# Optimization experiments

Hardware: AMD Instinct MI355X
Metric: run time of the kernel (lower is better)

## Reference

```python
import jax, jax.numpy as jnp
import numpy as np

B, S, D, H = 4, 2048, 1024, 16
DH = D // H


def setup_inputs() -> dict:
    key = jax.random.key(0)
    k1, k2, k3 = jax.random.split(key, 3)
    x = jax.random.normal(k1, (B, S, D), dtype=jnp.float32)
    w_attn = jax.random.normal(k2, (D, 3 * D), dtype=jnp.float32) * 0.02
    b_attn = jnp.zeros((3 * D,), dtype=jnp.float32)
    w_proj = jax.random.normal(k3, (D, D), dtype=jnp.float32) * 0.02
    b_proj = jnp.zeros((D,), dtype=jnp.float32)
    return {"x": x, "w_attn": w_attn, "b_attn": b_attn, "w_proj": w_proj, "b_proj": b_proj}


def _split_heads(t):
    # [B, S, D] -> [B, H, S, DH]
    return t.reshape(B, S, H, DH).transpose(0, 2, 1, 3)


def reference(x, w_attn, b_attn, w_proj, b_proj):
    # fused QKV projection (TFConv1D = x @ w + b)
    qkv = jnp.einsum('bsd,df->bsf', x, w_attn) + b_attn  # [B, S, 3D]
    q, k, v = jnp.split(qkv, 3, axis=2)
    q, k, v = _split_heads(q), _split_heads(k), _split_heads(v)  # [B,H,S,DH]

    # scaled scores
    w = jnp.einsum('bhqd,bhkd->bhqk', q, k) / jnp.sqrt(jnp.asarray(DH, dtype=q.dtype))

    # causal mask: multiply + additive -10000 trick, as in original
    i = jnp.arange(S)[:, None]
    j = jnp.arange(S)[None, :]
    b = (i >= j).astype(w.dtype)  # nd == ns so i >= j - ns + nd == i >= j
    b = b[None, None]  # [1,1,S,S]
    w = w * b - 10000.0 * (1.0 - b)

    w = jax.nn.softmax(w, axis=-1)
    # attn_pdrop = 0.0 -> dropout is identity (eval)

    a = jnp.einsum('bhqk,bhkd->bhqd', w, v)  # [B,H,S,DH]
    a = a.transpose(0, 2, 1, 3).reshape(B, S, D)  # merge heads
    a = jnp.einsum('bsd,df->bsf', a, w_proj) + b_proj
    # resid_pdrop = 0.0 -> identity
    return a
```

## Files before the change

### kernel.cpp

```cpp
#include <hip/hip_runtime.h>
#include <stdint.h>

typedef __bf16 bf16x8 __attribute__((ext_vector_type(8)));
typedef float  f32x4  __attribute__((ext_vector_type(4)));

#define DEV __device__ __forceinline__

constexpr int Bc = 4, S = 2048, D = 1024, Hh = 16, DH = 64;
constexpr int Kdim = 1024;

DEV unsigned short f2bf(float f) {
    uint32_t u = __builtin_bit_cast(uint32_t, f);
    u += 0x7fff + ((u >> 16) & 1);
    return (unsigned short)(u >> 16);
}
DEV bf16x8 ld8(const unsigned short* p) {
    uint4 u = *(const uint4*)p;
    return __builtin_bit_cast(bf16x8, u);
}
DEV uint4 pack8(float4 a, float4 b) {
    union { uint4 u; unsigned short s[8]; } r;
    r.s[0] = f2bf(a.x); r.s[1] = f2bf(a.y); r.s[2] = f2bf(a.z); r.s[3] = f2bf(a.w);
    r.s[4] = f2bf(b.x); r.s[5] = f2bf(b.y); r.s[6] = f2bf(b.z); r.s[7] = f2bf(b.w);
    return r.u;
}

DEV void gl16(const void* g, void* l) {
    __builtin_amdgcn_global_load_lds((__attribute__((address_space(1))) void*)g,
                                     (__attribute__((address_space(3))) void*)l,
                                     16, 0, 0);
}

__global__ __launch_bounds__(256) void transpose_cvt(const float* __restrict__ in,
                                                     unsigned short* __restrict__ out,
                                                     int rows, int cols) {
    __shared__ float t[32][33];
    int tx = threadIdx.x & 31, ty = threadIdx.x >> 5;
    int c = blockIdx.x * 32 + tx;
    int rbase = blockIdx.y * 32;
    for (int rr = 0; rr < 32; rr += 8)
        t[ty + rr][tx] = in[(size_t)(rbase + ty + rr) * cols + c];
    __syncthreads();
    int orbase = blockIdx.x * 32;
    for (int rr = 0; rr < 32; rr += 8)
        out[(size_t)(orbase + ty + rr) * rows + rbase + tx] = f2bf(t[tx][ty + rr]);
}

__global__ __launch_bounds__(256) void cvt_bf16(const float* __restrict__ in,
                                                unsigned short* __restrict__ out) {
    size_t i = (size_t)blockIdx.x * 256 + threadIdx.x;
    const float4* p = (const float4*)(in + i * 8);
    float4 a = p[0], b = p[1];
    *(uint4*)(out + i * 8) = pack8(a, b);
}

__global__ __launch_bounds__(256) void gemm_bt(const unsigned short* __restrict__ A,
                                               const unsigned short* __restrict__ Bt,
                                               const float* __restrict__ bias,
                                               int mode,
                                               unsigned short* __restrict__ qo,
                                               unsigned short* __restrict__ ko,
                                               unsigned short* __restrict__ vo,
                                               float* __restrict__ outf) {
    __shared__ __align__(16) unsigned short As[128 * 64];
    __shared__ __align__(16) unsigned short Bs[128 * 64];
    const int tid = threadIdx.x;
    const int wave = tid >> 6, lane = tid & 63, g = lane >> 4, ln = lane & 15;
    const int wm = wave >> 1, wn = wave & 1;
    const int nwg = gridDim.x * gridDim.y;
    const int orig = blockIdx.y * gridDim.x + blockIdx.x;
    const int swz = (orig & 7) * (nwg >> 3) + (orig >> 3);
    const int m0 = (swz / gridDim.x) * 128, n0 = (swz % gridDim.x) * 128;

    f32x4 acc[4][4];
    for (int i = 0; i < 4; i++)
        for (int j = 0; j < 4; j++) acc[i][j] = f32x4{0.f, 0.f, 0.f, 0.f};

    for (int k0 = 0; k0 < Kdim; k0 += 64) {
#pragma unroll
        for (int c = 0; c < 4; c++) {
            int L = c * 4096 + tid * 16;
            int row = L >> 7;
            int colb = (L & 127) ^ ((row & 7) << 4);
            gl16((const char*)A  + ((size_t)(m0 + row) * Kdim + k0) * 2 + colb,
                 (char*)As + c * 4096 + wave * 1024);
            gl16((const char*)Bt + ((size_t)(n0 + row) * Kdim + k0) * 2 + colb,
                 (char*)Bs + c * 4096 + wave * 1024);
        }
        __syncthreads();
#pragma unroll
        for (int kk = 0; kk < 2; kk++) {
            bf16x8 af[4], bfr[4];
#pragma unroll
            for (int t = 0; t < 4; t++) {
                int ra = wm * 64 + t * 16 + ln;
                int rb = wn * 64 + t * 16 + ln;
                int co = kk * 64 + g * 16;
                af[t]  = ld8((const unsigned short*)((const char*)As + ra * 128 + (co ^ ((ra & 7) << 4))));
                bfr[t] = ld8((const unsigned short*)((const char*)Bs + rb * 128 + (co ^ ((rb & 7) << 4))));
            }
#pragma unroll
            for (int mt = 0; mt < 4; mt++)
#pragma unroll
                for (int nt = 0; nt < 4; nt++)
                    acc[mt][nt] = __builtin_amdgcn_mfma_f32_16x16x32_bf16(af[mt], bfr[nt], acc[mt][nt], 0, 0, 0);
        }
        __syncthreads();
    }

    for (int mt = 0; mt < 4; mt++)
        for (int nt = 0; nt < 4; nt++)
            for (int r = 0; r < 4; r++) {
                int m = m0 + wm * 64 + mt * 16 + g * 4 + r;
                int n = n0 + wn * 64 + nt * 16 + ln;
                float val = acc[mt][nt][r] + bias[n];
                if (mode == 0) {
                    int which = n >> 10, rem = n & 1023;
                    int hh = rem >> 6, dd = rem & 63;
                    int b = m >> 11, s = m & 2047;
                    int bh = (b << 4) + hh;
                    if (which == 0)      qo[((size_t)bh * S + s) * DH + dd] = f2bf(val);
                    else if (which == 1) ko[((size_t)bh * S + s) * DH + dd] = f2bf(val);
                    else                 vo[((size_t)bh * DH + dd) * S + s] = f2bf(val);
                } else {
                    outf[(size_t)m * 1024 + n] = val;
                }
            }
}

__global__ __launch_bounds__(256, 3) void attn_fwd(const unsigned short* __restrict__ qg,
                                                   const unsigned short* __restrict__ kg,
                                                   const unsigned short* __restrict__ vtg,
                                                   unsigned short* __restrict__ og) {
    __shared__ __align__(16) unsigned short Ks[128 * 64];
    __shared__ __align__(16) unsigned short Vs[64 * 128];
    __shared__ __align__(16) unsigned short P [64 * 136];
    const int idx = blockIdx.x;
    const int qt = 31 - (idx >> 6);
    const int bh = idx & 63;
    const int b = bh >> 4, h = bh & 15;
    const size_t base = (size_t)bh * S * DH;
    const unsigned short* qp = qg + base;
    const char* kpb  = (const char*)(kg  + base);
    const char* vtpb = (const char*)(vtg + base);
    const int tid = threadIdx.x, wave = tid >> 6, lane = tid & 63;
    const int g = lane >> 4, ln = lane & 15;
    const int q0 = qt * 64, wq = wave * 16;
    const int jn = (qt >> 1) + 1;

    bf16x8 qf[2];
    qf[0] = ld8(qp + (size_t)(q0 + wq + ln) * DH + g * 8);
    qf[1] = ld8(qp + (size_t)(q0 + wq + ln) * DH + 32 + g * 8);

    f32x4 o_t[4];
#pragma unroll
    for (int dt = 0; dt < 4; dt++) o_t[dt] = f32x4{0.f, 0.f, 0.f, 0.f};
    float m_ = -1e30f, l_ = 0.f;

#pragma unroll 1
    for (int j = 0; j < jn; j++) {
        const char* kj = kpb + (size_t)j * (128 * DH * 2);
        const char* vj = vtpb + j * 256;
#pragma unroll
        for (int c = 0; c < 4; c++) {
            int L = c * 4096 + tid * 16;
            int kr = L >> 7, kcb = L & 127;
            gl16(kj + (size_t)kr * 128 + (kcb ^ ((kr & 7) << 4)),
                 (char*)Ks + c * 4096 + wave * 1024);
            int vr = L >> 8, vcb = L & 255;
            gl16(vj + (size_t)vr * 4096 + (vcb ^ ((vr & 15) << 4)),
                 (char*)Vs + c * 4096 + wave * 1024);
        }
        __syncthreads();

        f32x4 st[8];
#pragma unroll
        for (int mt = 0; mt < 8; mt++) {
            int row = mt * 16 + ln;
            int sw = (row & 7) << 4;
            const char* kb2 = (const char*)Ks + row * 128;
            bf16x8 kf0 = ld8((const unsigned short*)(kb2 + ((g * 16) ^ sw)));
            bf16x8 kf1 = ld8((const unsigned short*)(kb2 + ((64 + g * 16) ^ sw)));
            f32x4 t = f32x4{0.f, 0.f, 0.f, 0.f};
            t = __builtin_amdgcn_mfma_f32_16x16x32_bf16(kf0, qf[0], t, 0, 0, 0);
            t = __builtin_amdgcn_mfma_f32_16x16x32_bf16(kf1, qf[1], t, 0, 0, 0);
            st[mt] = t;
        }
        if (j == jn - 1) {
            int qgl = q0 + wq + ln;
#pragma unroll
            for (int mt = 0; mt < 8; mt++)
#pragma unroll
                for (int r = 0; r < 4; r++) {
                    int kvg = j * 128 + mt * 16 + g * 4 + r;
                    if (kvg > qgl) st[mt][r] = -3e38f;
                }
        }
        f32x4 mm = st[0];
#pragma unroll
        for (int mt = 1; mt < 8; mt++)
#pragma unroll
            for (int e = 0; e < 4; e++) mm[e] = fmaxf(mm[e], st[mt][e]);
        float mx = fmaxf(fmaxf(mm[0], mm[1]), fmaxf(mm[2], mm[3]));
        mx = fmaxf(mx, __shfl_xor(mx, 16));
        mx = fmaxf(mx, __shfl_xor(mx, 32));
        float mnew = fmaxf(m_, mx);
        float alpha = __expf((m_ - mnew) * 0.125f);
        f32x4 sv = f32x4{0.f, 0.f, 0.f, 0.f};
#pragma unroll
        for (int mt = 0; mt < 8; mt++) {
            f32x4 pr;
#pragma unroll
            for (int e = 0; e < 4; e++) pr[e] = __expf((st[mt][e] - mnew) * 0.125f);
            st[mt] = pr;
            sv += pr;
        }
        float rs = (sv[0] + sv[1]) + (sv[2] + sv[3]);
        rs += __shfl_xor(rs, 16);
        rs += __shfl_xor(rs, 32);
        l_ = l_ * alpha + rs;
        m_ = mnew;

#pragma unroll
        for (int mt = 0; mt < 8; mt++) {
            uint4 u = __builtin_bit_cast(uint4, st[mt]);
            uint2 w;
            w.x = (u.y & 0xFFFF0000u) | (u.x >> 16);
            w.y = (u.w & 0xFFFF0000u) | (u.z >> 16);
            *(uint2*)&P[(wq + ln) * 136 + mt * 16 + g * 4] = w;
        }
#pragma unroll
        for (int dt = 0; dt < 4; dt++) o_t[dt] *= alpha;

#pragma unroll
        for (int kc = 0; kc < 4; kc++) {
            bf16x8 pf = ld8(&P[(wq + ln) * 136 + kc * 32 + g * 8]);
            bf16x8 vf[4];
#pragma unroll
            for (int dt = 0; dt < 4; dt++) {
                int row = dt * 16 + ln;
                vf[dt] = ld8((const unsigned short*)((const char*)Vs + row * 256 +
                             ((kc * 64 + g * 16) ^ ((row & 15) << 4))));
            }
#pragma unroll
            for (int dt = 0; dt < 4; dt++)
                o_t[dt] = __builtin_amdgcn_mfma_f32_16x16x32_bf16(vf[dt], pf, o_t[dt], 0, 0, 0);
        }
        __syncthreads();
    }

    float il = 1.f / l_;
#pragma unroll
    for (int dt = 0; dt < 4; dt++) o_t[dt] *= il;
    float* Ot = (float*)&P[wq * 136];
#pragma unroll
    for (int dt = 0; dt < 4; dt++)
        *(float4*)&Ot[ln * 68 + dt * 16 + g * 4] =
            float4{o_t[dt][0], o_t[dt][1], o_t[dt][2], o_t[dt][3]};
#pragma unroll
    for (int i = 0; i < 4; i++) {
        float4 v = *(float4*)&Ot[(i * 4 + g) * 68 + ln * 4];
        uint2 w;
        w.x = (uint32_t)f2bf(v.x) | ((uint32_t)f2bf(v.y) << 16);
        w.y = (uint32_t)f2bf(v.z) | ((uint32_t)f2bf(v.w) << 16);
        *(uint2*)&og[((size_t)(b * S + q0 + wq + i * 4 + g)) * D + h * DH + ln * 4] = w;
    }
}

extern "C" void kernel_launch(void* const* d_in, const int* in_sizes, int n_in,
                              void* d_out, int out_size, void* d_ws, size_t ws_size,
                              hipStream_t stream) {
    (void)in_sizes; (void)n_in; (void)out_size; (void)ws_size;
    const float* x      = (const float*)d_in[0];
    const float* w_attn = (const float*)d_in[1];
    const float* b_attn = (const float*)d_in[2];
    const float* w_proj = (const float*)d_in[3];
    const float* b_proj = (const float*)d_in[4];

    char* ws = (char*)d_ws;
    unsigned short* wattn_t = (unsigned short*)ws;
    unsigned short* wproj_t = (unsigned short*)(ws + 6291456);
    unsigned short* xb      = (unsigned short*)(ws + 8388608);
    unsigned short* qb      = (unsigned short*)(ws + 25165824);
    unsigned short* kb      = (unsigned short*)(ws + 41943040);
    unsigned short* vtb     = (unsigned short*)(ws + 58720256);
    unsigned short* aob     = (unsigned short*)(ws + 75497472);

    transpose_cvt<<<dim3(96, 32), 256, 0, stream>>>(w_attn, wattn_t, 1024, 3072);
    transpose_cvt<<<dim3(32, 32), 256, 0, stream>>>(w_proj, wproj_t, 1024, 1024);
    cvt_bf16<<<dim3(4096), 256, 0, stream>>>(x, xb);
    gemm_bt<<<dim3(24, 64), 256, 0, stream>>>(xb, wattn_t, b_attn, 0, qb, kb, vtb, nullptr);
    attn_fwd<<<dim3(2048), 256, 0, stream>>>(qb, kb, vtb, aob);
    gemm_bt<<<dim3(8, 64), 256, 0, stream>>>(aob, wproj_t, b_proj, 1,
                                             nullptr, nullptr, nullptr, (float*)d_out);
}
```

Measured before the change: 284.0 us.

## Double-buffer GEMM LDS tiles and widen attention blocks to 128 queries

The GEMM kernel now keeps two LDS buffers and issues the global-to-LDS loads for the next K slice before computing on the current one. This hides load latency behind the MFMAs and leaves one barrier per iteration. The attention kernel moves to 512 threads with 128-row query tiles, so each K/V tile load is shared by twice as many queries and the grid is halved. The costs are doubled LDS use in the GEMM, a larger P buffer, fewer attention blocks, and coarser causal tiles that may compute more masked work.

```diff
diff --git a/kernel.cpp b/kernel.cpp
--- a/kernel.cpp
+++ b/kernel.cpp
@@ -62,8 +62,8 @@
                                                unsigned short* __restrict__ ko,
                                                unsigned short* __restrict__ vo,
                                                float* __restrict__ outf) {
-    __shared__ __align__(16) unsigned short As[128 * 64];
-    __shared__ __align__(16) unsigned short Bs[128 * 64];
+    __shared__ __align__(16) unsigned short As[2][128 * 64];
+    __shared__ __align__(16) unsigned short Bs[2][128 * 64];
     const int tid = threadIdx.x;
     const int wave = tid >> 6, lane = tid & 63, g = lane >> 4, ln = lane & 15;
     const int wm = wave >> 1, wn = wave & 1;
@@ -76,28 +76,39 @@
     for (int i = 0; i < 4; i++)
         for (int j = 0; j < 4; j++) acc[i][j] = f32x4{0.f, 0.f, 0.f, 0.f};
 
-    for (int k0 = 0; k0 < Kdim; k0 += 64) {
-#pragma unroll
-        for (int c = 0; c < 4; c++) {
-            int L = c * 4096 + tid * 16;
-            int row = L >> 7;
-            int colb = (L & 127) ^ ((row & 7) << 4);
-            gl16((const char*)A  + ((size_t)(m0 + row) * Kdim + k0) * 2 + colb,
-                 (char*)As + c * 4096 + wave * 1024);
-            gl16((const char*)Bt + ((size_t)(n0 + row) * Kdim + k0) * 2 + colb,
-                 (char*)Bs + c * 4096 + wave * 1024);
-        }
-        __syncthreads();
+#define STAGE_G(buf, k0)                                                            \
+    _Pragma("unroll")                                                               \
+    for (int c = 0; c < 4; c++) {                                                   \
+        int L = c * 4096 + tid * 16;                                                \
+        int row = L >> 7;                                                           \
+        int colb = (L & 127) ^ ((row & 7) << 4);                                    \
+        gl16((const char*)A  + ((size_t)(m0 + row) * Kdim + (k0)) * 2 + colb,       \
+             (char*)As[buf] + c * 4096 + wave * 1024);                              \
+        gl16((const char*)Bt + ((size_t)(n0 + row) * Kdim + (k0)) * 2 + colb,       \
+             (char*)Bs[buf] + c * 4096 + wave * 1024);                              \
+    }
+
+    STAGE_G(0, 0);
+    asm volatile("s_waitcnt vmcnt(0)" ::: "memory");
+    __builtin_amdgcn_s_barrier();
+    asm volatile("" ::: "memory");
+
+#pragma unroll 1
+    for (int t = 0; t < 16; t++) {
+        const int buf = t & 1;
+        if (t + 1 < 16) STAGE_G(buf ^ 1, (t + 1) * 64);
+        const unsigned short* Asb = As[buf];
+        const unsigned short* Bsb = Bs[buf];
 #pragma unroll
         for (int kk = 0; kk < 2; kk++) {
             bf16x8 af[4], bfr[4];
 #pragma unroll
-            for (int t = 0; t < 4; t++) {
-                int ra = wm * 64 + t * 16 + ln;
-                int rb = wn * 64 + t * 16 + ln;
+            for (int u = 0; u < 4; u++) {
+                int ra = wm * 64 + u * 16 + ln;
+                int rb = wn * 64 + u * 16 + ln;
                 int co = kk * 64 + g * 16;
-                af[t]  = ld8((const unsigned short*)((const char*)As + ra * 128 + (co ^ ((ra & 7) << 4))));
-                bfr[t] = ld8((const unsigned short*)((const char*)Bs + rb * 128 + (co ^ ((rb & 7) << 4))));
+                af[u]  = ld8((const unsigned short*)((const char*)Asb + ra * 128 + (co ^ ((ra & 7) << 4))));
+                bfr[u] = ld8((const unsigned short*)((const char*)Bsb + rb * 128 + (co ^ ((rb & 7) << 4))));
             }
 #pragma unroll
             for (int mt = 0; mt < 4; mt++)
@@ -105,8 +116,12 @@
                 for (int nt = 0; nt < 4; nt++)
                     acc[mt][nt] = __builtin_amdgcn_mfma_f32_16x16x32_bf16(af[mt], bfr[nt], acc[mt][nt], 0, 0, 0);
         }
-        __syncthreads();
+        asm volatile("" ::: "memory");
+        asm volatile("s_waitcnt vmcnt(0)" ::: "memory");
+        __builtin_amdgcn_s_barrier();
+        asm volatile("" ::: "memory");
     }
+#undef STAGE_G
 
     for (int mt = 0; mt < 4; mt++)
         for (int nt = 0; nt < 4; nt++)
@@ -128,15 +143,15 @@
             }
 }
 
-__global__ __launch_bounds__(256, 3) void attn_fwd(const unsigned short* __restrict__ qg,
+__global__ __launch_bounds__(512, 4) void attn_fwd(const unsigned short* __restrict__ qg,
                                                    const unsigned short* __restrict__ kg,
                                                    const unsigned short* __restrict__ vtg,
                                                    unsigned short* __restrict__ og) {
     __shared__ __align__(16) unsigned short Ks[128 * 64];
     __shared__ __align__(16) unsigned short Vs[64 * 128];
-    __shared__ __align__(16) unsigned short P [64 * 136];
+    __shared__ __align__(16) unsigned short P [128 * 136];
     const int idx = blockIdx.x;
-    const int qt = 31 - (idx >> 6);
+    const int qt = 15 - (idx >> 6);
     const int bh = idx & 63;
     const int b = bh >> 4, h = bh & 15;
     const size_t base = (size_t)bh * S * DH;
@@ -145,8 +160,8 @@
     const char* vtpb = (const char*)(vtg + base);
     const int tid = threadIdx.x, wave = tid >> 6, lane = tid & 63;
     const int g = lane >> 4, ln = lane & 15;
-    const int q0 = qt * 64, wq = wave * 16;
-    const int jn = (qt >> 1) + 1;
+    const int q0 = qt * 128, wq = wave * 16;
+    const int jn = qt + 1;
 
     bf16x8 qf[2];
     qf[0] = ld8(qp + (size_t)(q0 + wq + ln) * DH + g * 8);
@@ -162,14 +177,14 @@
         const char* kj = kpb + (size_t)j * (128 * DH * 2);
         const char* vj = vtpb + j * 256;
 #pragma unroll
-        for (int c = 0; c < 4; c++) {
-            int L = c * 4096 + tid * 16;
+        for (int c = 0; c < 2; c++) {
+            int L = c * 8192 + tid * 16;
             int kr = L >> 7, kcb = L & 127;
             gl16(kj + (size_t)kr * 128 + (kcb ^ ((kr & 7) << 4)),
-                 (char*)Ks + c * 4096 + wave * 1024);
+                 (char*)Ks + c * 8192 + wave * 1024);
             int vr = L >> 8, vcb = L & 255;
             gl16(vj + (size_t)vr * 4096 + (vcb ^ ((vr & 15) << 4)),
-                 (char*)Vs + c * 4096 + wave * 1024);
+                 (char*)Vs + c * 8192 + wave * 1024);
         }
         __syncthreads();
 
@@ -290,7 +305,7 @@
     transpose_cvt<<<dim3(32, 32), 256, 0, stream>>>(w_proj, wproj_t, 1024, 1024);
     cvt_bf16<<<dim3(4096), 256, 0, stream>>>(x, xb);
     gemm_bt<<<dim3(24, 64), 256, 0, stream>>>(xb, wattn_t, b_attn, 0, qb, kb, vtb, nullptr);
-    attn_fwd<<<dim3(2048), 256, 0, stream>>>(qb, kb, vtb, aob);
+    attn_fwd<<<dim3(1024), 512, 0, stream>>>(qb, kb, vtb, aob);
     gemm_bt<<<dim3(8, 64), 256, 0, stream>>>(aob, wproj_t, b_proj, 1,
                                              nullptr, nullptr, nullptr, (float*)d_out);
 }
```

Result: faster. 264.5 us (-6.9%).
